# Kernel optimization log

Hardware: AMD Instinct MI355X
Metric: run time of the kernel (lower is better)

The kernel has to match this reference:

```python
import jax, jax.numpy as jnp
import numpy as np

N = 100000          # number of nodes (nums)
E = 1200000         # nnz of the normalized adjacency
D = 64              # embed_size; layer_size = [64, 64, 64]
NODE_DROP = 0.1     # args.node_dropout[0]
MESS_DROP = (0.1, 0.1, 0.1)
EPS = 1e-12         # F.normalize eps


def setup_inputs() -> dict:
    key = jax.random.key(0)
    ks = jax.random.split(key, 10)
    rows = jax.random.randint(ks[0], (E,), 0, N, dtype=jnp.int32)
    cols = jax.random.randint(ks[1], (E,), 0, N, dtype=jnp.int32)
    vals = jax.random.uniform(ks[2], (E,), dtype=jnp.float32)
    emb = jax.random.normal(ks[3], (N, D), dtype=jnp.float32) * 0.1
    W0 = jax.random.normal(ks[4], (D, D), dtype=jnp.float32) * 0.1
    b0 = jax.random.normal(ks[5], (1, D), dtype=jnp.float32) * 0.1
    W1 = jax.random.normal(ks[6], (D, D), dtype=jnp.float32) * 0.1
    b1 = jax.random.normal(ks[7], (1, D), dtype=jnp.float32) * 0.1
    W2 = jax.random.normal(ks[8], (D, D), dtype=jnp.float32) * 0.1
    b2 = jax.random.normal(ks[9], (1, D), dtype=jnp.float32) * 0.1
    return dict(rows=rows, cols=cols, vals=vals, emb=emb,
                W0=W0, b0=b0, W1=W1, b1=b1, W2=W2, b2=b2)


def reference(rows, cols, vals, emb, W0, b0, W1, b1, W2, b2):
    drop_key = jax.random.key(42)
    k_node, k0, k1, k2 = jax.random.split(drop_key, 4)

    # sparse node dropout: zero dropped edge values (== removing nnz), scale survivors
    keep_e = jax.random.bernoulli(k_node, 1.0 - NODE_DROP, (E,))
    a_vals = jnp.where(keep_e, vals / (1.0 - NODE_DROP), 0.0)

    def layer(ego, W, b, rate, k):
        # SpMM: out[r] += a_vals * ego[c]   (COO scatter-add)
        side = jax.ops.segment_sum(a_vals[:, None] * ego[cols], rows, num_segments=N)
        h = side @ W + b
        keep = jax.random.bernoulli(k, 1.0 - rate, h.shape)
        h = jnp.where(keep, h / (1.0 - rate), 0.0)          # mess dropout
        nrm = h / jnp.maximum(jnp.linalg.norm(h, axis=1, keepdims=True), EPS)
        return h, nrm  # ego continues as the (un-normalized) dropped output

    all_embs = [emb]
    ego = emb
    for (W, b, rate, k) in ((W0, b0, MESS_DROP[0], k0),
                            (W1, b1, MESS_DROP[1], k1),
                            (W2, b2, MESS_DROP[2], k2)):
        ego, nrm = layer(ego, W, b, rate, k)
        all_embs.append(nrm)
    return jnp.concatenate(all_embs, axis=1)  # [N, 4*D]
```

## Files before the change

kernel.cpp:

```cpp
#include <hip/hip_runtime.h>
#include <stdint.h>

#define N_NODES 100000
#define DIM 64
#define E_EDGES 1200000
#define NBK 6250
#define NREP 8
#define BCAP_R 64
#define ROW_CAP 40
#define BPB 16

__host__ __device__ __forceinline__ void tf2x32(uint32_t k0, uint32_t k1,
                                                uint32_t c0, uint32_t c1,
                                                uint32_t& o0, uint32_t& o1) {
    uint32_t ks2 = k0 ^ k1 ^ 0x1BD11BDAu;
    uint32_t x0 = c0 + k0, x1 = c1 + k1;
#define TF_RND(r) { x0 += x1; x1 = (x1 << r) | (x1 >> (32 - r)); x1 ^= x0; }
    TF_RND(13) TF_RND(15) TF_RND(26) TF_RND(6)
    x0 += k1;  x1 += ks2 + 1u;
    TF_RND(17) TF_RND(29) TF_RND(16) TF_RND(24)
    x0 += ks2; x1 += k0 + 2u;
    TF_RND(13) TF_RND(15) TF_RND(26) TF_RND(6)
    x0 += k0;  x1 += k1 + 3u;
    TF_RND(17) TF_RND(29) TF_RND(16) TF_RND(24)
    x0 += k1;  x1 += ks2 + 4u;
    TF_RND(13) TF_RND(15) TF_RND(26) TF_RND(6)
    x0 += ks2; x1 += k0 + 5u;
#undef TF_RND
    o0 = x0; o1 = x1;
}

__device__ __forceinline__ bool keep_bit(uint32_t k0, uint32_t k1, uint32_t idx) {
    uint32_t y0, y1;
    tf2x32(k0, k1, 0u, idx, y0, y1);
    return (((y0 ^ y1) >> 9) < 7549747u);
}

__device__ __forceinline__ uint16_t f2bf(float f) {
    uint32_t x = __float_as_uint(f);
    return (uint16_t)((x + 0x7fffu + ((x >> 16) & 1u)) >> 16);
}

__global__ void k_embcvt(const float* __restrict__ emb, float* __restrict__ out,
                         uint16_t* __restrict__ egoA, int* __restrict__ bcnt) {
    int gid = blockIdx.x * blockDim.x + threadIdx.x;
    if (gid < NREP * NBK) bcnt[gid] = 0;
    int stride = gridDim.x * blockDim.x;
    const int total = N_NODES * 16;
    for (int i = gid; i < total; i += stride) {
        int n = i >> 4, q = i & 15;
        float4 v = ((const float4*)emb)[(size_t)n * 16 + q];
        ((float4*)out)[(size_t)n * 64 + q] = v;
        ushort4 bb;
        bb.x = f2bf(v.x); bb.y = f2bf(v.y); bb.z = f2bf(v.z); bb.w = f2bf(v.w);
        ((ushort4*)egoA)[(size_t)n * 16 + q] = bb;
    }
}

__global__ void k_bucket(const int* __restrict__ rows, const int* __restrict__ cols,
                         const float* __restrict__ vals, int* __restrict__ bcnt,
                         int2* __restrict__ bedge, uint32_t k0, uint32_t k1) {
    int rep = blockIdx.x & (NREP - 1);
    int i = blockIdx.x * blockDim.x + threadIdx.x;
    int stride = gridDim.x * blockDim.x;
    for (; i < E_EDGES; i += stride) {
        if (keep_bit(k0, k1, (uint32_t)i)) {
            int r = rows[i];
            int b = r >> 4;
            int rl = r & 15;
            int cell = rep * NBK + b;
            int pos = atomicAdd(&bcnt[cell], 1);
            if (pos < BCAP_R)
                bedge[(size_t)cell * BCAP_R + pos] =
                    make_int2((rl << 17) | cols[i],
                              __float_as_int(vals[i] * (1.0f / 0.9f)));
        }
    }
}

__global__ __launch_bounds__(256) void k_bin(const int2* __restrict__ bedge,
                                             const int* __restrict__ bcnt,
                                             uint32_t* __restrict__ pairs,
                                             int* __restrict__ cnt) {
    __shared__ uint32_t lp[256 * ROW_CAP];
    __shared__ int lc[256];
    __shared__ int lcc[BPB * NREP];
    int blk = blockIdx.x, t = threadIdx.x;
    for (int i = t; i < 256 * ROW_CAP / 4; i += 256)
        ((uint4*)lp)[i] = make_uint4(0u, 0u, 0u, 0u);
    lc[t] = 0;
    int b0 = blk * BPB;
    if (t < BPB * NREP) {
        int lb = t >> 3, rep = t & 7;
        int ne = bcnt[rep * NBK + b0 + lb];
        lcc[t] = (ne > BCAP_R) ? BCAP_R : ne;
    }
    __syncthreads();
    int e = t & 63, wv = t >> 6;
    for (int cc = 0; cc < BPB * NREP; cc += 4) {
        int cell = cc + wv;
        int lb = cell >> 3, rep = cell & 7;
        int ne = lcc[cell];
        if (e < ne) {
            int2 en = bedge[((size_t)(rep * NBK + b0 + lb)) * BCAP_R + e];
            uint32_t meta = (uint32_t)en.x;
            int rl = (int)(meta >> 17);
            uint32_t col = meta & 0x1FFFFu;
            float v = __int_as_float(en.y);
            int rloc = lb * 16 + rl;
            int pos = atomicAdd(&lc[rloc], 1);
            if (pos < ROW_CAP) {
                uint32_t q = (uint32_t)(v * 16384.0f + 0.5f);
                lp[rloc * ROW_CAP + pos] = (q << 17) | col;
            }
        }
    }
    __syncthreads();
    int nrows = N_NODES - blk * 256;
    if (nrows > 256) nrows = 256;
    int nq = nrows * ROW_CAP / 4;
    uint4* dst = (uint4*)(pairs + (size_t)blk * 256 * ROW_CAP);
    const uint4* src = (const uint4*)lp;
    for (int i = t; i < nq; i += 256) dst[i] = src[i];
    if (t < nrows) cnt[blk * 256 + t] = lc[t];
}

#define GATHER_FMA(V, aE, aO)                                              \
    {                                                                      \
        uint32_t c0 = V.x & 0x1FFFFu;  float a0 = (float)(V.x >> 17) * S;  \
        uint32_t c1 = V.y & 0x1FFFFu;  float a1 = (float)(V.y >> 17) * S;  \
        uint32_t c2 = V.z & 0x1FFFFu;  float a2 = (float)(V.z >> 17) * S;  \
        uint32_t c3 = V.w & 0x1FFFFu;  float a3 = (float)(V.w >> 17) * S;  \
        uint32_t u0 = egoU[c0 * 32u + (uint32_t)l2];                       \
        uint32_t u1 = egoU[c1 * 32u + (uint32_t)l2];                       \
        uint32_t u2 = egoU[c2 * 32u + (uint32_t)l2];                       \
        uint32_t u3 = egoU[c3 * 32u + (uint32_t)l2];                       \
        aE = fmaf(a0, __uint_as_float(u0 << 16), aE);                      \
        aO = fmaf(a0, __uint_as_float(u0 & 0xffff0000u), aO);              \
        aE = fmaf(a1, __uint_as_float(u1 << 16), aE);                      \
        aO = fmaf(a1, __uint_as_float(u1 & 0xffff0000u), aO);              \
        aE = fmaf(a2, __uint_as_float(u2 << 16), aE);                      \
        aO = fmaf(a2, __uint_as_float(u2 & 0xffff0000u), aO);              \
        aE = fmaf(a3, __uint_as_float(u3 << 16), aE);                      \
        aO = fmaf(a3, __uint_as_float(u3 & 0xffff0000u), aO);              \
    }

__global__ __launch_bounds__(256, 3) void k_layer(
    const int* __restrict__ cnt, const uint32_t* __restrict__ pairs,
    const uint16_t* __restrict__ ego_in,
    uint16_t* __restrict__ h_out,
    float* __restrict__ out, int coloff,
    const float* __restrict__ W, const float* __restrict__ bias,
    uint32_t k0, uint32_t k1) {
    __shared__ float sS[16][64];
    int t = threadIdx.x;
    int w = t >> 6, lane = t & 63;

    float wreg[64];
#pragma unroll
    for (int k = 0; k < 64; ++k)
        wreg[k] = W[k * 64 + lane];
    float breg = bias[lane];

    const float S = 1.0f / 16384.0f;
    int l2 = lane & 31;
    int hiSel = lane >> 5;
    int hi4 = hiSel << 2;
    const uint32_t* egoU = (const uint32_t*)ego_in;
    int wid0 = blockIdx.x * 4 + w;
    const int NW = 2048 * 4;
    const int NQ = N_NODES / 4;
    for (int q = wid0; q < NQ; q += NW) {
        int un = __builtin_amdgcn_readfirstlane(q * 4);
        int len0 = (cnt[un + 0] + 7) & ~7;  if (len0 > ROW_CAP) len0 = ROW_CAP;
        int len1 = (cnt[un + 1] + 7) & ~7;  if (len1 > ROW_CAP) len1 = ROW_CAP;
        int len2 = (cnt[un + 2] + 7) & ~7;  if (len2 > ROW_CAP) len2 = ROW_CAP;
        int len3 = (cnt[un + 3] + 7) & ~7;  if (len3 > ROW_CAP) len3 = ROW_CAP;
        const uint32_t* rp = pairs + (size_t)un * ROW_CAP + hi4;
        float aE0 = 0.f, aO0 = 0.f, aE1 = 0.f, aO1 = 0.f;
        float aE2 = 0.f, aO2 = 0.f, aE3 = 0.f, aO3 = 0.f;
        int jmax = len0;
        if (len1 > jmax) jmax = len1;
        if (len2 > jmax) jmax = len2;
        if (len3 > jmax) jmax = len3;
        const uint4 zed = make_uint4(0u, 0u, 0u, 0u);
        for (int j = 0; j < jmax; j += 8) {
            uint4 V0 = (j < len0) ? *reinterpret_cast<const uint4*>(rp + j) : zed;
            uint4 V1 = (j < len1) ? *reinterpret_cast<const uint4*>(rp + ROW_CAP + j) : zed;
            uint4 V2 = (j < len2) ? *reinterpret_cast<const uint4*>(rp + 2 * ROW_CAP + j) : zed;
            uint4 V3 = (j < len3) ? *reinterpret_cast<const uint4*>(rp + 3 * ROW_CAP + j) : zed;
            GATHER_FMA(V0, aE0, aO0)
            GATHER_FMA(V1, aE1, aO1)
            GATHER_FMA(V2, aE2, aO2)
            GATHER_FMA(V3, aE3, aO3)
        }
        aE0 += __shfl_xor(aE0, 32, 64);  aO0 += __shfl_xor(aO0, 32, 64);
        aE1 += __shfl_xor(aE1, 32, 64);  aO1 += __shfl_xor(aO1, 32, 64);
        aE2 += __shfl_xor(aE2, 32, 64);  aO2 += __shfl_xor(aO2, 32, 64);
        aE3 += __shfl_xor(aE3, 32, 64);  aO3 += __shfl_xor(aO3, 32, 64);
        float2 vA = hiSel ? make_float2(aE2, aO2) : make_float2(aE0, aO0);
        float2 vB = hiSel ? make_float2(aE3, aO3) : make_float2(aE1, aO1);
        reinterpret_cast<float2*>(&sS[4 * w + 2 * hiSel][0])[l2] = vA;
        reinterpret_cast<float2*>(&sS[4 * w + 2 * hiSel + 1][0])[l2] = vB;
        float h0 = breg, h1 = breg, h2 = breg, h3 = breg;
        const float4* s0p = reinterpret_cast<const float4*>(&sS[4 * w + 0][0]);
        const float4* s1p = reinterpret_cast<const float4*>(&sS[4 * w + 1][0]);
        const float4* s2p = reinterpret_cast<const float4*>(&sS[4 * w + 2][0]);
        const float4* s3p = reinterpret_cast<const float4*>(&sS[4 * w + 3][0]);
#pragma unroll
        for (int kq = 0; kq < 16; ++kq) {
            float4 s0 = s0p[kq], s1 = s1p[kq], s2 = s2p[kq], s3 = s3p[kq];
            float w0 = wreg[4 * kq + 0], w1 = wreg[4 * kq + 1];
            float w2 = wreg[4 * kq + 2], w3 = wreg[4 * kq + 3];
            h0 = fmaf(s0.x, w0, h0); h1 = fmaf(s1.x, w0, h1);
            h2 = fmaf(s2.x, w0, h2); h3 = fmaf(s3.x, w0, h3);
            h0 = fmaf(s0.y, w1, h0); h1 = fmaf(s1.y, w1, h1);
            h2 = fmaf(s2.y, w1, h2); h3 = fmaf(s3.y, w1, h3);
            h0 = fmaf(s0.z, w2, h0); h1 = fmaf(s1.z, w2, h1);
            h2 = fmaf(s2.z, w2, h2); h3 = fmaf(s3.z, w2, h3);
            h0 = fmaf(s0.w, w3, h0); h1 = fmaf(s1.w, w3, h1);
            h2 = fmaf(s2.w, w3, h2); h3 = fmaf(s3.w, w3, h3);
        }
        uint32_t base_idx = (uint32_t)un * 64u + (uint32_t)lane;
        h0 = keep_bit(k0, k1, base_idx)        ? h0 * (1.0f / 0.9f) : 0.0f;
        h1 = keep_bit(k0, k1, base_idx + 64u)  ? h1 * (1.0f / 0.9f) : 0.0f;
        h2 = keep_bit(k0, k1, base_idx + 128u) ? h2 * (1.0f / 0.9f) : 0.0f;
        h3 = keep_bit(k0, k1, base_idx + 192u) ? h3 * (1.0f / 0.9f) : 0.0f;
        float s0 = h0 * h0, s1 = h1 * h1, s2 = h2 * h2, s3 = h3 * h3;
#pragma unroll
        for (int o = 32; o > 0; o >>= 1) {
            s0 += __shfl_xor(s0, o, 64);
            s1 += __shfl_xor(s1, o, 64);
            s2 += __shfl_xor(s2, o, 64);
            s3 += __shfl_xor(s3, o, 64);
        }
        float nv0 = h0 / fmaxf(sqrtf(s0), 1e-12f);
        float nv1 = h1 / fmaxf(sqrtf(s1), 1e-12f);
        float nv2 = h2 / fmaxf(sqrtf(s2), 1e-12f);
        float nv3 = h3 / fmaxf(sqrtf(s3), 1e-12f);
        if (h_out) {
            h_out[(size_t)(un + 0) * DIM + lane] = f2bf(h0);
            h_out[(size_t)(un + 1) * DIM + lane] = f2bf(h1);
            h_out[(size_t)(un + 2) * DIM + lane] = f2bf(h2);
            h_out[(size_t)(un + 3) * DIM + lane] = f2bf(h3);
        }
        out[(size_t)(un + 0) * 256 + coloff + lane] = nv0;
        out[(size_t)(un + 1) * 256 + coloff + lane] = nv1;
        out[(size_t)(un + 2) * 256 + coloff + lane] = nv2;
        out[(size_t)(un + 3) * 256 + coloff + lane] = nv3;
    }
}

extern "C" void kernel_launch(void* const* d_in, const int* in_sizes, int n_in,
                              void* d_out, int out_size, void* d_ws, size_t ws_size,
                              hipStream_t stream) {
    const int*   rows = (const int*)d_in[0];
    const int*   cols = (const int*)d_in[1];
    const float* vals = (const float*)d_in[2];
    const float* emb  = (const float*)d_in[3];
    const float* Wk[3] = { (const float*)d_in[4], (const float*)d_in[6], (const float*)d_in[8] };
    const float* bk[3] = { (const float*)d_in[5], (const float*)d_in[7], (const float*)d_in[9] };
    float* out = (float*)d_out;

    int*      bcnt  = (int*)d_ws;
    int*      cnt   = bcnt + 65536;
    int2*     bedge = (int2*)(cnt + 100000 + 14);
    bedge = (int2*)(((uintptr_t)bedge + 511) & ~(uintptr_t)511);
    uint32_t* pairs = (uint32_t*)(bedge + (size_t)NREP * NBK * BCAP_R);
    uint16_t* egoA  = (uint16_t*)(pairs + (size_t)N_NODES * ROW_CAP);
    uint16_t* egoB  = egoA + (size_t)N_NODES * DIM;

    uint32_t kn[2], kl[3][2];
    tf2x32(0u, 42u, 0u, 0u, kn[0], kn[1]);
    tf2x32(0u, 42u, 0u, 1u, kl[0][0], kl[0][1]);
    tf2x32(0u, 42u, 0u, 2u, kl[1][0], kl[1][1]);
    tf2x32(0u, 42u, 0u, 3u, kl[2][0], kl[2][1]);

    k_embcvt<<<2048, 256, 0, stream>>>(emb, out, egoA, bcnt);
    k_bucket<<<2048, 256, 0, stream>>>(rows, cols, vals, bcnt, bedge, kn[0], kn[1]);
    k_bin<<<(NBK + BPB - 1) / BPB, 256, 0, stream>>>(bedge, bcnt, pairs, cnt);

    k_layer<<<2048, 256, 0, stream>>>(cnt, pairs, egoA, egoB, out, 64,
                                      Wk[0], bk[0], kl[0][0], kl[0][1]);
    k_layer<<<2048, 256, 0, stream>>>(cnt, pairs, egoB, egoA, out, 128,
                                      Wk[1], bk[1], kl[1][0], kl[1][1]);
    k_layer<<<2048, 256, 0, stream>>>(cnt, pairs, egoA, nullptr, out, 192,
                                      Wk[2], bk[2], kl[2][0], kl[2][1]);
}
```

Before: 257.5 us.

## Split fused layer kernel into SpMM and dense epilogue kernels via fp32 side buffer

The fused per-layer kernel is split in two. One SpMM kernel gathers neighbour embeddings and writes fp32 aggregates to a workspace side buffer. A separate epilogue kernel does the 64x64 matmul, bias, dropout, normalization and output writes. This frees the SpMM kernel from holding 64 weight registers so it can run at higher occupancy (launch bounds raised to 6). The first 16 edges per row are also loaded unconditionally, to issue gather loads earlier. The cost is an extra round trip of N*64 floats per layer and three more kernel launches.

Measured after the change: 256.2 us. Within noise of the previous version (-0.5%).

```diff
diff --git a/kernel.cpp b/kernel.cpp
--- a/kernel.cpp
+++ b/kernel.cpp
@@ -145,109 +145,110 @@
         aO = fmaf(a3, __uint_as_float(u3 & 0xffff0000u), aO);              \
     }
 
-__global__ __launch_bounds__(256, 3) void k_layer(
+__global__ __launch_bounds__(256, 6) void k_spmm(
     const int* __restrict__ cnt, const uint32_t* __restrict__ pairs,
-    const uint16_t* __restrict__ ego_in,
-    uint16_t* __restrict__ h_out,
-    float* __restrict__ out, int coloff,
-    const float* __restrict__ W, const float* __restrict__ bias,
-    uint32_t k0, uint32_t k1) {
-    __shared__ float sS[16][64];
+    const uint16_t* __restrict__ ego_in, float* __restrict__ side) {
     int t = threadIdx.x;
     int w = t >> 6, lane = t & 63;
-
-    float wreg[64];
-#pragma unroll
-    for (int k = 0; k < 64; ++k)
-        wreg[k] = W[k * 64 + lane];
-    float breg = bias[lane];
-
+    int l2 = lane & 31;
+    int hi4 = (lane >> 5) << 2;
     const float S = 1.0f / 16384.0f;
-    int l2 = lane & 31;
-    int hiSel = lane >> 5;
-    int hi4 = hiSel << 2;
     const uint32_t* egoU = (const uint32_t*)ego_in;
     int wid0 = blockIdx.x * 4 + w;
     const int NW = 2048 * 4;
     const int NQ = N_NODES / 4;
     for (int q = wid0; q < NQ; q += NW) {
         int un = __builtin_amdgcn_readfirstlane(q * 4);
-        int len0 = (cnt[un + 0] + 7) & ~7;  if (len0 > ROW_CAP) len0 = ROW_CAP;
-        int len1 = (cnt[un + 1] + 7) & ~7;  if (len1 > ROW_CAP) len1 = ROW_CAP;
-        int len2 = (cnt[un + 2] + 7) & ~7;  if (len2 > ROW_CAP) len2 = ROW_CAP;
-        int len3 = (cnt[un + 3] + 7) & ~7;  if (len3 > ROW_CAP) len3 = ROW_CAP;
+        int l0 = cnt[un + 0], l1 = cnt[un + 1], l2c = cnt[un + 2], l3 = cnt[un + 3];
         const uint32_t* rp = pairs + (size_t)un * ROW_CAP + hi4;
+        uint4 A0 = *reinterpret_cast<const uint4*>(rp);
+        uint4 A1 = *reinterpret_cast<const uint4*>(rp + ROW_CAP);
+        uint4 A2 = *reinterpret_cast<const uint4*>(rp + 2 * ROW_CAP);
+        uint4 A3 = *reinterpret_cast<const uint4*>(rp + 3 * ROW_CAP);
+        uint4 B0 = *reinterpret_cast<const uint4*>(rp + 8);
+        uint4 B1 = *reinterpret_cast<const uint4*>(rp + ROW_CAP + 8);
+        uint4 B2 = *reinterpret_cast<const uint4*>(rp + 2 * ROW_CAP + 8);
+        uint4 B3 = *reinterpret_cast<const uint4*>(rp + 3 * ROW_CAP + 8);
         float aE0 = 0.f, aO0 = 0.f, aE1 = 0.f, aO1 = 0.f;
         float aE2 = 0.f, aO2 = 0.f, aE3 = 0.f, aO3 = 0.f;
-        int jmax = len0;
-        if (len1 > jmax) jmax = len1;
-        if (len2 > jmax) jmax = len2;
-        if (len3 > jmax) jmax = len3;
-        const uint4 zed = make_uint4(0u, 0u, 0u, 0u);
-        for (int j = 0; j < jmax; j += 8) {
-            uint4 V0 = (j < len0) ? *reinterpret_cast<const uint4*>(rp + j) : zed;
-            uint4 V1 = (j < len1) ? *reinterpret_cast<const uint4*>(rp + ROW_CAP + j) : zed;
-            uint4 V2 = (j < len2) ? *reinterpret_cast<const uint4*>(rp + 2 * ROW_CAP + j) : zed;
-            uint4 V3 = (j < len3) ? *reinterpret_cast<const uint4*>(rp + 3 * ROW_CAP + j) : zed;
-            GATHER_FMA(V0, aE0, aO0)
-            GATHER_FMA(V1, aE1, aO1)
-            GATHER_FMA(V2, aE2, aO2)
-            GATHER_FMA(V3, aE3, aO3)
+        GATHER_FMA(A0, aE0, aO0)
+        GATHER_FMA(A1, aE1, aO1)
+        GATHER_FMA(A2, aE2, aO2)
+        GATHER_FMA(A3, aE3, aO3)
+        GATHER_FMA(B0, aE0, aO0)
+        GATHER_FMA(B1, aE1, aO1)
+        GATHER_FMA(B2, aE2, aO2)
+        GATHER_FMA(B3, aE3, aO3)
+        int n0 = (l0 + 7) & ~7;  if (n0 > ROW_CAP) n0 = ROW_CAP;
+        int n1 = (l1 + 7) & ~7;  if (n1 > ROW_CAP) n1 = ROW_CAP;
+        int n2 = (l2c + 7) & ~7; if (n2 > ROW_CAP) n2 = ROW_CAP;
+        int n3 = (l3 + 7) & ~7;  if (n3 > ROW_CAP) n3 = ROW_CAP;
+        int jmax = n0;
+        if (n1 > jmax) jmax = n1;
+        if (n2 > jmax) jmax = n2;
+        if (n3 > jmax) jmax = n3;
+        if (jmax > 16) {
+            const uint4 zed = make_uint4(0u, 0u, 0u, 0u);
+            for (int j = 16; j < jmax; j += 8) {
+                uint4 V0 = (j < n0) ? *reinterpret_cast<const uint4*>(rp + j) : zed;
+                uint4 V1 = (j < n1) ? *reinterpret_cast<const uint4*>(rp + ROW_CAP + j) : zed;
+                uint4 V2 = (j < n2) ? *reinterpret_cast<const uint4*>(rp + 2 * ROW_CAP + j) : zed;
+                uint4 V3 = (j < n3) ? *reinterpret_cast<const uint4*>(rp + 3 * ROW_CAP + j) : zed;
+                GATHER_FMA(V0, aE0, aO0)
+                GATHER_FMA(V1, aE1, aO1)
+                GATHER_FMA(V2, aE2, aO2)
+                GATHER_FMA(V3, aE3, aO3)
+            }
         }
         aE0 += __shfl_xor(aE0, 32, 64);  aO0 += __shfl_xor(aO0, 32, 64);
         aE1 += __shfl_xor(aE1, 32, 64);  aO1 += __shfl_xor(aO1, 32, 64);
         aE2 += __shfl_xor(aE2, 32, 64);  aO2 += __shfl_xor(aO2, 32, 64);
         aE3 += __shfl_xor(aE3, 32, 64);  aO3 += __shfl_xor(aO3, 32, 64);
-        float2 vA = hiSel ? make_float2(aE2, aO2) : make_float2(aE0, aO0);
-        float2 vB = hiSel ? make_float2(aE3, aO3) : make_float2(aE1, aO1);
-        reinterpret_cast<float2*>(&sS[4 * w + 2 * hiSel][0])[l2] = vA;
-        reinterpret_cast<float2*>(&sS[4 * w + 2 * hiSel + 1][0])[l2] = vB;
-        float h0 = breg, h1 = breg, h2 = breg, h3 = breg;
-        const float4* s0p = reinterpret_cast<const float4*>(&sS[4 * w + 0][0]);
-        const float4* s1p = reinterpret_cast<const float4*>(&sS[4 * w + 1][0]);
-        const float4* s2p = reinterpret_cast<const float4*>(&sS[4 * w + 2][0]);
-        const float4* s3p = reinterpret_cast<const float4*>(&sS[4 * w + 3][0]);
+        int nsel = (lane >> 5) * 2;
+        float2 vA = (lane < 32) ? make_float2(aE0, aO0) : make_float2(aE2, aO2);
+        float2 vB = (lane < 32) ? make_float2(aE1, aO1) : make_float2(aE3, aO3);
+        reinterpret_cast<float2*>(side + (size_t)(un + nsel) * DIM)[l2] = vA;
+        reinterpret_cast<float2*>(side + (size_t)(un + nsel + 1) * DIM)[l2] = vB;
+    }
+}
+
+__global__ __launch_bounds__(256, 4) void k_epi(
+    const float* __restrict__ side,
+    const float* __restrict__ W, const float* __restrict__ bias,
+    uint16_t* __restrict__ h_out,
+    float* __restrict__ out, int coloff,
+    uint32_t k0, uint32_t k1) {
+    __shared__ float sS[4][64];
+    int t = threadIdx.x;
+    int w = t >> 6, lane = t & 63;
+    float wreg[64];
+#pragma unroll
+    for (int k = 0; k < 64; ++k)
+        wreg[k] = W[k * 64 + lane];
+    float breg = bias[lane];
+    int wid0 = blockIdx.x * 4 + w;
+    const int NW = 2048 * 4;
+    for (int n = wid0; n < N_NODES; n += NW) {
+        int un = __builtin_amdgcn_readfirstlane(n);
+        float acc = side[(size_t)un * DIM + lane];
+        sS[w][lane] = acc;
+        float h = breg;
+        const float4* s4p = reinterpret_cast<const float4*>(&sS[w][0]);
 #pragma unroll
         for (int kq = 0; kq < 16; ++kq) {
-            float4 s0 = s0p[kq], s1 = s1p[kq], s2 = s2p[kq], s3 = s3p[kq];
-            float w0 = wreg[4 * kq + 0], w1 = wreg[4 * kq + 1];
-            float w2 = wreg[4 * kq + 2], w3 = wreg[4 * kq + 3];
-            h0 = fmaf(s0.x, w0, h0); h1 = fmaf(s1.x, w0, h1);
-            h2 = fmaf(s2.x, w0, h2); h3 = fmaf(s3.x, w0, h3);
-            h0 = fmaf(s0.y, w1, h0); h1 = fmaf(s1.y, w1, h1);
-            h2 = fmaf(s2.y, w1, h2); h3 = fmaf(s3.y, w1, h3);
-            h0 = fmaf(s0.z, w2, h0); h1 = fmaf(s1.z, w2, h1);
-            h2 = fmaf(s2.z, w2, h2); h3 = fmaf(s3.z, w2, h3);
-            h0 = fmaf(s0.w, w3, h0); h1 = fmaf(s1.w, w3, h1);
-            h2 = fmaf(s2.w, w3, h2); h3 = fmaf(s3.w, w3, h3);
-        }
-        uint32_t base_idx = (uint32_t)un * 64u + (uint32_t)lane;
-        h0 = keep_bit(k0, k1, base_idx)        ? h0 * (1.0f / 0.9f) : 0.0f;
-        h1 = keep_bit(k0, k1, base_idx + 64u)  ? h1 * (1.0f / 0.9f) : 0.0f;
-        h2 = keep_bit(k0, k1, base_idx + 128u) ? h2 * (1.0f / 0.9f) : 0.0f;
-        h3 = keep_bit(k0, k1, base_idx + 192u) ? h3 * (1.0f / 0.9f) : 0.0f;
-        float s0 = h0 * h0, s1 = h1 * h1, s2 = h2 * h2, s3 = h3 * h3;
+            float4 s4 = s4p[kq];
+            h = fmaf(s4.x, wreg[4 * kq + 0], h);
+            h = fmaf(s4.y, wreg[4 * kq + 1], h);
+            h = fmaf(s4.z, wreg[4 * kq + 2], h);
+            h = fmaf(s4.w, wreg[4 * kq + 3], h);
+        }
+        h = keep_bit(k0, k1, (uint32_t)un * 64u + (uint32_t)lane) ? h * (1.0f / 0.9f) : 0.0f;
+        float s = h * h;
 #pragma unroll
-        for (int o = 32; o > 0; o >>= 1) {
-            s0 += __shfl_xor(s0, o, 64);
-            s1 += __shfl_xor(s1, o, 64);
-            s2 += __shfl_xor(s2, o, 64);
-            s3 += __shfl_xor(s3, o, 64);
-        }
-        float nv0 = h0 / fmaxf(sqrtf(s0), 1e-12f);
-        float nv1 = h1 / fmaxf(sqrtf(s1), 1e-12f);
-        float nv2 = h2 / fmaxf(sqrtf(s2), 1e-12f);
-        float nv3 = h3 / fmaxf(sqrtf(s3), 1e-12f);
-        if (h_out) {
-            h_out[(size_t)(un + 0) * DIM + lane] = f2bf(h0);
-            h_out[(size_t)(un + 1) * DIM + lane] = f2bf(h1);
-            h_out[(size_t)(un + 2) * DIM + lane] = f2bf(h2);
-            h_out[(size_t)(un + 3) * DIM + lane] = f2bf(h3);
-        }
-        out[(size_t)(un + 0) * 256 + coloff + lane] = nv0;
-        out[(size_t)(un + 1) * 256 + coloff + lane] = nv1;
-        out[(size_t)(un + 2) * 256 + coloff + lane] = nv2;
-        out[(size_t)(un + 3) * 256 + coloff + lane] = nv3;
+        for (int o = 32; o > 0; o >>= 1) s += __shfl_xor(s, o, 64);
+        float nv = h / fmaxf(sqrtf(s), 1e-12f);
+        if (h_out) h_out[(size_t)un * DIM + lane] = f2bf(h);
+        out[(size_t)un * 256 + coloff + lane] = nv;
     }
 }
 
@@ -267,7 +268,8 @@
     int2*     bedge = (int2*)(cnt + 100000 + 14);
     bedge = (int2*)(((uintptr_t)bedge + 511) & ~(uintptr_t)511);
     uint32_t* pairs = (uint32_t*)(bedge + (size_t)NREP * NBK * BCAP_R);
-    uint16_t* egoA  = (uint16_t*)(pairs + (size_t)N_NODES * ROW_CAP);
+    float*    side  = (float*)(pairs + (size_t)N_NODES * ROW_CAP);
+    uint16_t* egoA  = (uint16_t*)(side + (size_t)N_NODES * DIM);
     uint16_t* egoB  = egoA + (size_t)N_NODES * DIM;
 
     uint32_t kn[2], kl[3][2];
@@ -280,10 +282,13 @@
     k_bucket<<<2048, 256, 0, stream>>>(rows, cols, vals, bcnt, bedge, kn[0], kn[1]);
     k_bin<<<(NBK + BPB - 1) / BPB, 256, 0, stream>>>(bedge, bcnt, pairs, cnt);
 
-    k_layer<<<2048, 256, 0, stream>>>(cnt, pairs, egoA, egoB, out, 64,
-                                      Wk[0], bk[0], kl[0][0], kl[0][1]);
-    k_layer<<<2048, 256, 0, stream>>>(cnt, pairs, egoB, egoA, out, 128,
-                                      Wk[1], bk[1], kl[1][0], kl[1][1]);
-    k_layer<<<2048, 256, 0, stream>>>(cnt, pairs, egoA, nullptr, out, 192,
-                                      Wk[2], bk[2], kl[2][0], kl[2][1]);
-}
+    k_spmm<<<2048, 256, 0, stream>>>(cnt, pairs, egoA, side);
+    k_epi<<<2048, 256, 0, stream>>>(side, Wk[0], bk[0], egoB, out, 64,
+                                    kl[0][0], kl[0][1]);
+    k_spmm<<<2048, 256, 0, stream>>>(cnt, pairs, egoB, side);
+    k_epi<<<2048, 256, 0, stream>>>(side, Wk[1], bk[1], egoA, out, 128,
+                                    kl[1][0], kl[1][1]);
+    k_spmm<<<2048, 256, 0, stream>>>(cnt, pairs, egoA, side);
+    k_epi<<<2048, 256, 0, stream>>>(side, Wk[2], bk[2], nullptr, out, 192,
+                                    kl[2][0], kl[2][1]);
+}
```
